# Kernel tuning notes

Measured on AMD Instinct MI355X. Metric: run time of the kernel, lower is better.

## Reference

```python
import jax, jax.numpy as jnp
import numpy as np

N_NODES = 50000
N_EDGES = 800000
HIDDEN = 64
NUM_FEATURES = 1
OUT_DIM = 2


def setup_inputs() -> dict:
    key = jax.random.key(0)
    k = jax.random.split(key, 6)
    x = jax.random.normal(k[0], (N_NODES, NUM_FEATURES), dtype=jnp.float32)
    edge_index = jax.random.randint(k[1], (2, N_EDGES), 0, N_NODES, dtype=jnp.int32)
    # GCNConv params (PyG default: glorot weight, zero bias; random here for testing)
    W1 = jax.random.normal(k[2], (NUM_FEATURES, HIDDEN), dtype=jnp.float32) * 0.5
    b1 = jax.random.normal(k[3], (HIDDEN,), dtype=jnp.float32) * 0.1
    W2 = jax.random.normal(k[4], (HIDDEN, OUT_DIM), dtype=jnp.float32) * 0.1
    b2 = jax.random.normal(k[5], (OUT_DIM,), dtype=jnp.float32) * 0.1
    return {"x": x, "edge_index": edge_index, "W1": W1, "b1": b1, "W2": W2, "b2": b2}


def _gcn_norm(edge_index, num_nodes):
    # PyG gcn_norm with add_self_loops=True, symmetric normalization
    row, col = edge_index[0], edge_index[1]
    loop = jnp.arange(num_nodes, dtype=row.dtype)
    row = jnp.concatenate([row, loop])
    col = jnp.concatenate([col, loop])
    ew = jnp.ones(row.shape[0], dtype=jnp.float32)
    deg = jax.ops.segment_sum(ew, col, num_segments=num_nodes)  # in-degree incl. self-loop
    dinv = jnp.where(deg > 0, jax.lax.rsqrt(deg), 0.0)
    norm = dinv[row] * dinv[col]  # [E+N]
    return row, col, norm


def _gcn_conv(x, row, col, norm, W, b, num_nodes):
    h = x @ W                                  # [N, out] transform first (out <= in here is fine)
    msg = h[row] * norm[:, None]               # gather + scale, [E+N, out]
    out = jax.ops.segment_sum(msg, col, num_segments=num_nodes)  # scatter-add at targets
    return out + b


def reference(x, edge_index, W1, b1, W2, b2):
    row, col, norm = _gcn_norm(edge_index, N_NODES)
    h = _gcn_conv(x, row, col, norm, W1, b1, N_NODES)
    h = jax.nn.relu(h)
    out = _gcn_conv(h, row, col, norm, W2, b2, N_NODES)
    return out
```

## Files before the change

kernel.cpp:

```cpp
#include <hip/hip_runtime.h>
#include <math.h>

#define N_NODES 50000
#define N_EDGES 800000
#define HIDDEN  64
#define NPART   500
#define PCHUNK  1600
#define NBUCK   32
#define SLICE   1568
#define CAPB    128
#define BCAP    26000
#define NSUB    16


__global__ __launch_bounds__(256)
void k_part(const int* __restrict__ row, const int* __restrict__ col,
            unsigned* __restrict__ tails, unsigned* __restrict__ bks) {
    __shared__ unsigned stage[NBUCK * CAPB];
    __shared__ unsigned cnt2[NBUCK], gpos[NBUCK];
    const int t   = threadIdx.x;
    const int blk = blockIdx.x;
    const int e0  = blk * PCHUNK;
    if (t < NBUCK) cnt2[t] = 0u;
    __syncthreads();
    const int4* c4 = (const int4*)(col + e0);
    const int4* r4 = (const int4*)(row + e0);
    for (int i = t; i < PCHUNK / 4; i += 256) {
        int4 cv = c4[i];
        int4 rv = r4[i];
#pragma unroll
        for (int k = 0; k < 4; ++k) {
            int c = (&cv.x)[k], r = (&rv.x)[k];
            int b = c / SLICE;
            unsigned off = atomicAdd(&cnt2[b], 1u);
            if (off < CAPB)
                stage[(b << 7) + off] = ((unsigned)(c - b * SLICE) << 16) | (unsigned)r;
        }
    }
    __syncthreads();
    if (t < NBUCK) {
        unsigned cc = min(cnt2[t], (unsigned)CAPB);
        cnt2[t] = cc;
        gpos[t] = atomicAdd(&tails[t], cc);
    }
    __syncthreads();
    for (int i = t; i < NBUCK * CAPB; i += 256) {
        int b = i >> 7; unsigned o = (unsigned)(i & 127);
        if (o < cnt2[b]) {
            unsigned dst = gpos[b] + o;
            if (dst < BCAP) bks[(size_t)b * BCAP + dst] = stage[i];
        }
    }
}

__device__ __forceinline__ void sub_range(unsigned tail, int s, unsigned& lo, unsigned& hi) {
    unsigned chunk = ((tail + NSUB - 1) / NSUB + 3u) & ~3u;
    lo = s * chunk;
    hi = min(lo + chunk, tail);
    if (lo > tail) lo = tail;
}

__global__ __launch_bounds__(256)
void k_deg(const unsigned* __restrict__ tails, const unsigned* __restrict__ bks,
           unsigned* __restrict__ part_deg) {
    __shared__ unsigned acc[SLICE];
    const int b = blockIdx.x >> 4;
    const int s = blockIdx.x & (NSUB - 1);
    for (int i = threadIdx.x; i < SLICE; i += 256) acc[i] = 0u;
    __syncthreads();
    unsigned tail = min(tails[b], (unsigned)BCAP);
    unsigned lo, hi; sub_range(tail, s, lo, hi);
    const unsigned* bk = bks + (size_t)b * BCAP;
    const uint4* bk4 = (const uint4*)bk;
    unsigned hiv = hi & ~3u;
    for (unsigned i = (lo >> 2) + threadIdx.x; (i << 2) < hiv; i += 256) {
        uint4 v4 = bk4[i];
#pragma unroll
        for (int k = 0; k < 4; ++k) atomicAdd(&acc[(&v4.x)[k] >> 16], 1u);
    }
    for (unsigned i = hiv + threadIdx.x; i < hi; i += 256)
        atomicAdd(&acc[bk[i] >> 16], 1u);
    __syncthreads();
    unsigned* dst = part_deg + (size_t)blockIdx.x * SLICE;
    for (int i = threadIdx.x; i < SLICE; i += 256) dst[i] = acc[i];
}

__global__ __launch_bounds__(256)
void k_g(const unsigned* __restrict__ part_deg, const float* __restrict__ x,
         float* __restrict__ dinv, float* __restrict__ g) {
    int n = blockIdx.x * 256 + threadIdx.x;
    if (n >= N_NODES) return;
    int b = n / SLICE, cl = n - b * SLICE;
    const unsigned* p = part_deg + (size_t)b * NSUB * SLICE + cl;
    unsigned deg = 0;
#pragma unroll
    for (int s = 0; s < NSUB; ++s) deg += p[(size_t)s * SLICE];
    float di = rsqrtf((float)(deg + 1));
    dinv[n] = di;
    g[n] = di * x[n];
}

__global__ __launch_bounds__(256)
void k_agg1(const unsigned* __restrict__ tails, const unsigned* __restrict__ bks,
            const float* __restrict__ g, float* __restrict__ part1) {
    __shared__ float acc[SLICE];
    const int b = blockIdx.x >> 4;
    const int s = blockIdx.x & (NSUB - 1);
    for (int i = threadIdx.x; i < SLICE; i += 256) acc[i] = 0.0f;
    __syncthreads();
    unsigned tail = min(tails[b], (unsigned)BCAP);
    unsigned lo, hi; sub_range(tail, s, lo, hi);
    const unsigned* bk = bks + (size_t)b * BCAP;
    const uint4* bk4 = (const uint4*)bk;
    unsigned hiv = hi & ~3u;
    for (unsigned i = (lo >> 2) + threadIdx.x; (i << 2) < hiv; i += 256) {
        uint4 v4 = bk4[i];
        float g0 = g[v4.x & 0xFFFFu];
        float g1 = g[v4.y & 0xFFFFu];
        float g2 = g[v4.z & 0xFFFFu];
        float g3 = g[v4.w & 0xFFFFu];
        atomicAdd(&acc[v4.x >> 16], g0);
        atomicAdd(&acc[v4.y >> 16], g1);
        atomicAdd(&acc[v4.z >> 16], g2);
        atomicAdd(&acc[v4.w >> 16], g3);
    }
    for (unsigned i = hiv + threadIdx.x; i < hi; i += 256) {
        unsigned v = bk[i];
        atomicAdd(&acc[v >> 16], g[v & 0xFFFFu]);
    }
    __syncthreads();
    float* dst = part1 + (size_t)blockIdx.x * SLICE;
    for (int i = threadIdx.x; i < SLICE; i += 256) dst[i] = acc[i];
}

__global__ __launch_bounds__(256)
void k_mlp(const float* __restrict__ part1, const float* __restrict__ g,
           const float* __restrict__ dinv,
           const float* __restrict__ W1, const float* __restrict__ b1,
           const float* __restrict__ W2, float2* __restrict__ z) {
    int n = blockIdx.x * 256 + threadIdx.x;
    if (n >= N_NODES) return;
    int b = n / SLICE, cl = n - b * SLICE;
    const float* p = part1 + (size_t)b * NSUB * SLICE + cl;
    float t = 0.0f;
#pragma unroll
    for (int s = 0; s < NSUB; ++s) t += p[(size_t)s * SLICE];
    float di = dinv[n];
    float sv = di * (t + g[n]);
    float y0 = 0.0f, y1 = 0.0f;
#pragma unroll
    for (int k = 0; k < HIDDEN; ++k) {
        float h = fmaxf(sv * W1[k] + b1[k], 0.0f);
        y0 += h * W2[2 * k];
        y1 += h * W2[2 * k + 1];
    }
    z[n] = make_float2(di * y0, di * y1);
}

__global__ __launch_bounds__(256)
void k_agg2(const unsigned* __restrict__ tails, const unsigned* __restrict__ bks,
            const float2* __restrict__ z, float2* __restrict__ part2) {
    __shared__ float ax[SLICE];
    __shared__ float ay[SLICE];
    const int b = blockIdx.x >> 4;
    const int s = blockIdx.x & (NSUB - 1);
    for (int i = threadIdx.x; i < SLICE; i += 256) { ax[i] = 0.0f; ay[i] = 0.0f; }
    __syncthreads();
    unsigned tail = min(tails[b], (unsigned)BCAP);
    unsigned lo, hi; sub_range(tail, s, lo, hi);
    const unsigned* bk = bks + (size_t)b * BCAP;
    const uint4* bk4 = (const uint4*)bk;
    unsigned hiv = hi & ~3u;
    for (unsigned i = (lo >> 2) + threadIdx.x; (i << 2) < hiv; i += 256) {
        uint4 v4 = bk4[i];
        float2 z0 = z[v4.x & 0xFFFFu];
        float2 z1 = z[v4.y & 0xFFFFu];
        float2 z2 = z[v4.z & 0xFFFFu];
        float2 z3 = z[v4.w & 0xFFFFu];
        atomicAdd(&ax[v4.x >> 16], z0.x); atomicAdd(&ay[v4.x >> 16], z0.y);
        atomicAdd(&ax[v4.y >> 16], z1.x); atomicAdd(&ay[v4.y >> 16], z1.y);
        atomicAdd(&ax[v4.z >> 16], z2.x); atomicAdd(&ay[v4.z >> 16], z2.y);
        atomicAdd(&ax[v4.w >> 16], z3.x); atomicAdd(&ay[v4.w >> 16], z3.y);
    }
    for (unsigned i = hiv + threadIdx.x; i < hi; i += 256) {
        unsigned v = bk[i];
        float2 zz = z[v & 0xFFFFu];
        atomicAdd(&ax[v >> 16], zz.x);
        atomicAdd(&ay[v >> 16], zz.y);
    }
    __syncthreads();
    float2* dst = part2 + (size_t)blockIdx.x * SLICE;
    for (int i = threadIdx.x; i < SLICE; i += 256) dst[i] = make_float2(ax[i], ay[i]);
}

__global__ __launch_bounds__(256)
void k_final(const float2* __restrict__ part2, const float2* __restrict__ z,
             const float* __restrict__ dinv, const float* __restrict__ b2,
             float2* __restrict__ out) {
    int n = blockIdx.x * 256 + threadIdx.x;
    if (n >= N_NODES) return;
    int b = n / SLICE, cl = n - b * SLICE;
    const float2* p = part2 + (size_t)b * NSUB * SLICE + cl;
    float Tx = 0.0f, Ty = 0.0f;
#pragma unroll
    for (int s = 0; s < NSUB; ++s) {
        float2 v = p[(size_t)s * SLICE];
        Tx += v.x; Ty += v.y;
    }
    float di = dinv[n];
    float2 zn = z[n];
    out[n] = make_float2(di * (Tx + zn.x) + b2[0], di * (Ty + zn.y) + b2[1]);
}


extern "C" void kernel_launch(void* const* d_in, const int* in_sizes, int n_in,
                              void* d_out, int out_size, void* d_ws, size_t ws_size,
                              hipStream_t stream) {
    const float* x  = (const float*)d_in[0];
    const int*   ei = (const int*)d_in[1];
    const float* W1 = (const float*)d_in[2];
    const float* b1 = (const float*)d_in[3];
    const float* W2 = (const float*)d_in[4];
    const float* b2 = (const float*)d_in[5];

    const int* row = ei;
    const int* col = ei + N_EDGES;

    char* p = (char*)d_ws;
    unsigned* tails    = (unsigned*)p;  p += 128;
    unsigned* bks      = (unsigned*)p;  p += (size_t)NBUCK * BCAP * 4;
    unsigned* part_deg = (unsigned*)p;  p += (size_t)NBUCK * NSUB * SLICE * 4;
    float*    part1    = (float*)p;     p += (size_t)NBUCK * NSUB * SLICE * 4;
    float2*   part2    = (float2*)p;    p += (size_t)NBUCK * NSUB * SLICE * 8;
    float*    dinv     = (float*)p;     p += 200064;
    float*    g        = (float*)p;     p += 200064;
    float2*   z        = (float2*)p;

    const int gA = NBUCK * NSUB;
    const int gN = (N_NODES + 255) / 256;

    hipMemsetAsync(tails, 0, NBUCK * sizeof(unsigned), stream);
    k_part <<<NPART, 256, 0, stream>>>(row, col, tails, bks);
    k_deg  <<<gA,    256, 0, stream>>>(tails, bks, part_deg);
    k_g    <<<gN,    256, 0, stream>>>(part_deg, x, dinv, g);
    k_agg1 <<<gA,    256, 0, stream>>>(tails, bks, g, part1);
    k_mlp  <<<gN,    256, 0, stream>>>(part1, g, dinv, W1, b1, W2, z);
    k_agg2 <<<gA,    256, 0, stream>>>(tails, bks, z, part2);
    k_final<<<gN,    256, 0, stream>>>(part2, z, dinv, b2, (float2*)d_out);
}
```

Measured before the change: 112.0 us.

## Fuse per-node reduction kernels into aggregation kernels via last-block-done counters

Each edge-aggregation kernel now keeps a per-bucket atomic counter, and the last of the bucket's sub-blocks to finish reduces the partial slices for that bucket. This folds the separate k_g, k_mlp and k_final node kernels into the aggregation kernels, cutting seven launches to four and their inter-kernel gaps. The cost is extra threadfences and atomics, plus a serial tail where one block per bucket does the reduction and the MLP alone. The memset now covers the new counters.

```diff
diff --git a/kernel.cpp b/kernel.cpp
--- a/kernel.cpp
+++ b/kernel.cpp
@@ -60,60 +60,78 @@
     if (lo > tail) lo = tail;
 }
 
-__global__ __launch_bounds__(256)
-void k_deg(const unsigned* __restrict__ tails, const unsigned* __restrict__ bks,
-           unsigned* __restrict__ part_deg) {
+__device__ __forceinline__ bool last_block(unsigned* cnt, int b, unsigned* lastflag) {
+    __threadfence();
+    __syncthreads();
+    if (threadIdx.x == 0)
+        *lastflag = (atomicAdd(&cnt[b], 1u) == NSUB - 1u) ? 1u : 0u;
+    __syncthreads();
+    if (*lastflag == 0u) return false;
+    __threadfence();
+    return true;
+}
+
+__global__ __launch_bounds__(256)
+void k_degg(const unsigned* __restrict__ tails, const unsigned* __restrict__ bks,
+            unsigned* __restrict__ part_deg, unsigned* __restrict__ cnt,
+            const float* __restrict__ x, float* __restrict__ dinv, float* __restrict__ g) {
     __shared__ unsigned acc[SLICE];
+    __shared__ unsigned lastflag;
+    const int t = threadIdx.x;
     const int b = blockIdx.x >> 4;
     const int s = blockIdx.x & (NSUB - 1);
-    for (int i = threadIdx.x; i < SLICE; i += 256) acc[i] = 0u;
+    for (int i = t; i < SLICE; i += 256) acc[i] = 0u;
     __syncthreads();
     unsigned tail = min(tails[b], (unsigned)BCAP);
     unsigned lo, hi; sub_range(tail, s, lo, hi);
     const unsigned* bk = bks + (size_t)b * BCAP;
     const uint4* bk4 = (const uint4*)bk;
     unsigned hiv = hi & ~3u;
-    for (unsigned i = (lo >> 2) + threadIdx.x; (i << 2) < hiv; i += 256) {
+    for (unsigned i = (lo >> 2) + t; (i << 2) < hiv; i += 256) {
         uint4 v4 = bk4[i];
 #pragma unroll
         for (int k = 0; k < 4; ++k) atomicAdd(&acc[(&v4.x)[k] >> 16], 1u);
     }
-    for (unsigned i = hiv + threadIdx.x; i < hi; i += 256)
+    for (unsigned i = hiv + t; i < hi; i += 256)
         atomicAdd(&acc[bk[i] >> 16], 1u);
     __syncthreads();
     unsigned* dst = part_deg + (size_t)blockIdx.x * SLICE;
-    for (int i = threadIdx.x; i < SLICE; i += 256) dst[i] = acc[i];
-}
-
-__global__ __launch_bounds__(256)
-void k_g(const unsigned* __restrict__ part_deg, const float* __restrict__ x,
-         float* __restrict__ dinv, float* __restrict__ g) {
-    int n = blockIdx.x * 256 + threadIdx.x;
-    if (n >= N_NODES) return;
-    int b = n / SLICE, cl = n - b * SLICE;
-    const unsigned* p = part_deg + (size_t)b * NSUB * SLICE + cl;
-    unsigned deg = 0;
-#pragma unroll
-    for (int s = 0; s < NSUB; ++s) deg += p[(size_t)s * SLICE];
-    float di = rsqrtf((float)(deg + 1));
-    dinv[n] = di;
-    g[n] = di * x[n];
-}
-
-__global__ __launch_bounds__(256)
-void k_agg1(const unsigned* __restrict__ tails, const unsigned* __restrict__ bks,
-            const float* __restrict__ g, float* __restrict__ part1) {
+    for (int i = t; i < SLICE; i += 256) dst[i] = acc[i];
+
+    if (!last_block(cnt, b, &lastflag)) return;
+    const unsigned* pd = part_deg + (size_t)b * NSUB * SLICE;
+    for (int i = t; i < SLICE; i += 256) {
+        int n = b * SLICE + i;
+        if (n >= N_NODES) continue;
+        unsigned d = 0;
+#pragma unroll
+        for (int s2 = 0; s2 < NSUB; ++s2) d += pd[(size_t)s2 * SLICE + i];
+        float di = rsqrtf((float)(d + 1u));
+        dinv[n] = di;
+        g[n] = di * x[n];
+    }
+}
+
+__global__ __launch_bounds__(256)
+void k_agg1mlp(const unsigned* __restrict__ tails, const unsigned* __restrict__ bks,
+               const float* __restrict__ g, const float* __restrict__ dinv,
+               const float* __restrict__ W1, const float* __restrict__ b1,
+               const float* __restrict__ W2,
+               float* __restrict__ part1, unsigned* __restrict__ cnt,
+               float2* __restrict__ z) {
     __shared__ float acc[SLICE];
+    __shared__ unsigned lastflag;
+    const int t = threadIdx.x;
     const int b = blockIdx.x >> 4;
     const int s = blockIdx.x & (NSUB - 1);
-    for (int i = threadIdx.x; i < SLICE; i += 256) acc[i] = 0.0f;
+    for (int i = t; i < SLICE; i += 256) acc[i] = 0.0f;
     __syncthreads();
     unsigned tail = min(tails[b], (unsigned)BCAP);
     unsigned lo, hi; sub_range(tail, s, lo, hi);
     const unsigned* bk = bks + (size_t)b * BCAP;
     const uint4* bk4 = (const uint4*)bk;
     unsigned hiv = hi & ~3u;
-    for (unsigned i = (lo >> 2) + threadIdx.x; (i << 2) < hiv; i += 256) {
+    for (unsigned i = (lo >> 2) + t; (i << 2) < hiv; i += 256) {
         uint4 v4 = bk4[i];
         float g0 = g[v4.x & 0xFFFFu];
         float g1 = g[v4.y & 0xFFFFu];
@@ -124,54 +142,55 @@
         atomicAdd(&acc[v4.z >> 16], g2);
         atomicAdd(&acc[v4.w >> 16], g3);
     }
-    for (unsigned i = hiv + threadIdx.x; i < hi; i += 256) {
+    for (unsigned i = hiv + t; i < hi; i += 256) {
         unsigned v = bk[i];
         atomicAdd(&acc[v >> 16], g[v & 0xFFFFu]);
     }
     __syncthreads();
     float* dst = part1 + (size_t)blockIdx.x * SLICE;
-    for (int i = threadIdx.x; i < SLICE; i += 256) dst[i] = acc[i];
-}
-
-__global__ __launch_bounds__(256)
-void k_mlp(const float* __restrict__ part1, const float* __restrict__ g,
-           const float* __restrict__ dinv,
-           const float* __restrict__ W1, const float* __restrict__ b1,
-           const float* __restrict__ W2, float2* __restrict__ z) {
-    int n = blockIdx.x * 256 + threadIdx.x;
-    if (n >= N_NODES) return;
-    int b = n / SLICE, cl = n - b * SLICE;
-    const float* p = part1 + (size_t)b * NSUB * SLICE + cl;
-    float t = 0.0f;
-#pragma unroll
-    for (int s = 0; s < NSUB; ++s) t += p[(size_t)s * SLICE];
-    float di = dinv[n];
-    float sv = di * (t + g[n]);
-    float y0 = 0.0f, y1 = 0.0f;
-#pragma unroll
-    for (int k = 0; k < HIDDEN; ++k) {
-        float h = fmaxf(sv * W1[k] + b1[k], 0.0f);
-        y0 += h * W2[2 * k];
-        y1 += h * W2[2 * k + 1];
-    }
-    z[n] = make_float2(di * y0, di * y1);
-}
-
-__global__ __launch_bounds__(256)
-void k_agg2(const unsigned* __restrict__ tails, const unsigned* __restrict__ bks,
-            const float2* __restrict__ z, float2* __restrict__ part2) {
+    for (int i = t; i < SLICE; i += 256) dst[i] = acc[i];
+
+    if (!last_block(cnt, b, &lastflag)) return;
+    const float* p1 = part1 + (size_t)b * NSUB * SLICE;
+    for (int i = t; i < SLICE; i += 256) {
+        int n = b * SLICE + i;
+        if (n >= N_NODES) continue;
+        float tt = 0.0f;
+#pragma unroll
+        for (int s2 = 0; s2 < NSUB; ++s2) tt += p1[(size_t)s2 * SLICE + i];
+        float di = dinv[n];
+        float sv = di * (tt + g[n]);
+        float y0 = 0.0f, y1 = 0.0f;
+#pragma unroll
+        for (int k = 0; k < HIDDEN; ++k) {
+            float h = fmaxf(sv * W1[k] + b1[k], 0.0f);
+            y0 += h * W2[2 * k];
+            y1 += h * W2[2 * k + 1];
+        }
+        z[n] = make_float2(di * y0, di * y1);
+    }
+}
+
+__global__ __launch_bounds__(256)
+void k_agg2fin(const unsigned* __restrict__ tails, const unsigned* __restrict__ bks,
+               const float2* __restrict__ z, const float* __restrict__ dinv,
+               const float* __restrict__ b2,
+               float2* __restrict__ part2, unsigned* __restrict__ cnt,
+               float2* __restrict__ out) {
     __shared__ float ax[SLICE];
     __shared__ float ay[SLICE];
+    __shared__ unsigned lastflag;
+    const int t = threadIdx.x;
     const int b = blockIdx.x >> 4;
     const int s = blockIdx.x & (NSUB - 1);
-    for (int i = threadIdx.x; i < SLICE; i += 256) { ax[i] = 0.0f; ay[i] = 0.0f; }
+    for (int i = t; i < SLICE; i += 256) { ax[i] = 0.0f; ay[i] = 0.0f; }
     __syncthreads();
     unsigned tail = min(tails[b], (unsigned)BCAP);
     unsigned lo, hi; sub_range(tail, s, lo, hi);
     const unsigned* bk = bks + (size_t)b * BCAP;
     const uint4* bk4 = (const uint4*)bk;
     unsigned hiv = hi & ~3u;
-    for (unsigned i = (lo >> 2) + threadIdx.x; (i << 2) < hiv; i += 256) {
+    for (unsigned i = (lo >> 2) + t; (i << 2) < hiv; i += 256) {
         uint4 v4 = bk4[i];
         float2 z0 = z[v4.x & 0xFFFFu];
         float2 z1 = z[v4.y & 0xFFFFu];
@@ -182,7 +201,7 @@
         atomicAdd(&ax[v4.z >> 16], z2.x); atomicAdd(&ay[v4.z >> 16], z2.y);
         atomicAdd(&ax[v4.w >> 16], z3.x); atomicAdd(&ay[v4.w >> 16], z3.y);
     }
-    for (unsigned i = hiv + threadIdx.x; i < hi; i += 256) {
+    for (unsigned i = hiv + t; i < hi; i += 256) {
         unsigned v = bk[i];
         float2 zz = z[v & 0xFFFFu];
         atomicAdd(&ax[v >> 16], zz.x);
@@ -190,26 +209,23 @@
     }
     __syncthreads();
     float2* dst = part2 + (size_t)blockIdx.x * SLICE;
-    for (int i = threadIdx.x; i < SLICE; i += 256) dst[i] = make_float2(ax[i], ay[i]);
-}
-
-__global__ __launch_bounds__(256)
-void k_final(const float2* __restrict__ part2, const float2* __restrict__ z,
-             const float* __restrict__ dinv, const float* __restrict__ b2,
-             float2* __restrict__ out) {
-    int n = blockIdx.x * 256 + threadIdx.x;
-    if (n >= N_NODES) return;
-    int b = n / SLICE, cl = n - b * SLICE;
-    const float2* p = part2 + (size_t)b * NSUB * SLICE + cl;
-    float Tx = 0.0f, Ty = 0.0f;
-#pragma unroll
-    for (int s = 0; s < NSUB; ++s) {
-        float2 v = p[(size_t)s * SLICE];
-        Tx += v.x; Ty += v.y;
-    }
-    float di = dinv[n];
-    float2 zn = z[n];
-    out[n] = make_float2(di * (Tx + zn.x) + b2[0], di * (Ty + zn.y) + b2[1]);
+    for (int i = t; i < SLICE; i += 256) dst[i] = make_float2(ax[i], ay[i]);
+
+    if (!last_block(cnt, b, &lastflag)) return;
+    const float2* p2 = part2 + (size_t)b * NSUB * SLICE;
+    for (int i = t; i < SLICE; i += 256) {
+        int n = b * SLICE + i;
+        if (n >= N_NODES) continue;
+        float Tx = 0.0f, Ty = 0.0f;
+#pragma unroll
+        for (int s2 = 0; s2 < NSUB; ++s2) {
+            float2 v = p2[(size_t)s2 * SLICE + i];
+            Tx += v.x; Ty += v.y;
+        }
+        float di = dinv[n];
+        float2 zn = z[n];
+        out[n] = make_float2(di * (Tx + zn.x) + b2[0], di * (Ty + zn.y) + b2[1]);
+    }
 }
 
 
@@ -228,6 +244,9 @@
 
     char* p = (char*)d_ws;
     unsigned* tails    = (unsigned*)p;  p += 128;
+    unsigned* c_deg    = (unsigned*)p;  p += 128;
+    unsigned* c_a1     = (unsigned*)p;  p += 128;
+    unsigned* c_a2     = (unsigned*)p;  p += 128;
     unsigned* bks      = (unsigned*)p;  p += (size_t)NBUCK * BCAP * 4;
     unsigned* part_deg = (unsigned*)p;  p += (size_t)NBUCK * NSUB * SLICE * 4;
     float*    part1    = (float*)p;     p += (size_t)NBUCK * NSUB * SLICE * 4;
@@ -237,14 +256,10 @@
     float2*   z        = (float2*)p;
 
     const int gA = NBUCK * NSUB;
-    const int gN = (N_NODES + 255) / 256;
-
-    hipMemsetAsync(tails, 0, NBUCK * sizeof(unsigned), stream);
-    k_part <<<NPART, 256, 0, stream>>>(row, col, tails, bks);
-    k_deg  <<<gA,    256, 0, stream>>>(tails, bks, part_deg);
-    k_g    <<<gN,    256, 0, stream>>>(part_deg, x, dinv, g);
-    k_agg1 <<<gA,    256, 0, stream>>>(tails, bks, g, part1);
-    k_mlp  <<<gN,    256, 0, stream>>>(part1, g, dinv, W1, b1, W2, z);
-    k_agg2 <<<gA,    256, 0, stream>>>(tails, bks, z, part2);
-    k_final<<<gN,    256, 0, stream>>>(part2, z, dinv, b2, (float2*)d_out);
-}
+
+    hipMemsetAsync(tails, 0, 512, stream);
+    k_part   <<<NPART, 256, 0, stream>>>(row, col, tails, bks);
+    k_degg   <<<gA,    256, 0, stream>>>(tails, bks, part_deg, c_deg, x, dinv, g);
+    k_agg1mlp<<<gA,    256, 0, stream>>>(tails, bks, g, dinv, W1, b1, W2, part1, c_a1, z);
+    k_agg2fin<<<gA,    256, 0, stream>>>(tails, bks, z, dinv, b2, part2, c_a2, (float2*)d_out);
+}
```

After: 277.0 us. +147.3%, slower.
